# Optimization experiments

Measured on AMD Instinct MI355X. Metric: run time of the kernel, lower is better.

The kernel has to match this reference:

```python
import jax, jax.numpy as jnp
import numpy as np

NEG_INF = -1e30
LRELU_SLOPE = 0.2

B, E, IN_DIM, OUT_DIM = 64, 512, 1024, 256


def setup_inputs() -> dict:
    key = jax.random.key(0)
    ks = jax.random.split(key, 6)
    input_state = jax.random.normal(ks[0], (B, E, IN_DIM), dtype=jnp.float32)
    adj = jnp.ones((B, E, E), dtype=jnp.float32)  # only used via ones_like in the original
    node_mask = jax.random.randint(ks[1], (B, E, 1), 0, 2, dtype=jnp.int32)
    W_w = jax.random.normal(ks[2], (OUT_DIM, IN_DIM), dtype=jnp.float32) * (1.0 / np.sqrt(IN_DIM))
    W_b = jax.random.normal(ks[3], (OUT_DIM,), dtype=jnp.float32) * 0.02
    a_w = jax.random.normal(ks[4], (1, 2 * OUT_DIM), dtype=jnp.float32) * (1.0 / np.sqrt(2 * OUT_DIM))
    a_b = jax.random.normal(ks[5], (1,), dtype=jnp.float32) * 0.02
    return {"input_state": input_state, "adj": adj, "node_mask": node_mask,
            "W_w": W_w, "W_b": W_b, "a_w": a_w, "a_b": a_b}


def reference(input_state, adj, node_mask, W_w, W_b, a_w, a_b):
    # h = W(input_state); dropout is identity in eval mode (gnn_drop=0)
    h = jnp.einsum('bei,oi->beo', input_state, W_w) + W_b  # b,E,d
    d = h.shape[-1]
    # a([h_i ; h_j]) decomposes exactly: a_w[:, :d] @ h_i + a_w[:, d:] @ h_j + a_b
    a1, a2 = a_w[:, :d], a_w[:, d:]
    s1 = jnp.einsum('beo,xo->bex', h, a1)  # b,E,1 -> score contribution of source node i
    s2 = jnp.einsum('beo,xo->bex', h, a2)  # b,E,1 -> contribution of target node j
    scores = s1 + jnp.swapaxes(s2, 1, 2) + a_b  # b,E,E, scores[n,i,j] = a([h_i;h_j])
    scores = jnp.where(scores >= 0, scores, LRELU_SLOPE * scores)  # LeakyReLU(0.2)
    # fully-connected adjacency gated by node mask: mask_i * mask_j
    m = node_mask.astype(scores.dtype)  # b,E,1
    pair_mask = m * jnp.swapaxes(m, 1, 2)  # b,E,E
    scores = jnp.where(pair_mask > 0, scores, NEG_INF)
    coefs = jax.nn.softmax(scores, axis=-1)  # b,E,E
    h = h * m  # zero out masked nodes before aggregation
    return jnp.einsum('bij,bjo->bio', coefs, h)
```

## Files before the change

### kernel.cpp

```cpp
#include <hip/hip_runtime.h>
#include <hip/hip_fp16.h>
#include <math.h>

#define NEG_INF_F (-1e30f)
#define LRELU 0.2f

constexpr int Bb = 64, Ee = 512, IND = 1024, OUTD = 256;
constexpr int Mrows = Bb * Ee;

typedef __attribute__((ext_vector_type(8))) _Float16 half8;
typedef __attribute__((ext_vector_type(4))) _Float16 half4;
typedef __attribute__((ext_vector_type(4))) float floatx4;

#define AS1 __attribute__((address_space(1)))
#define AS3 __attribute__((address_space(3)))

__global__ __launch_bounds__(256) void wconv_kernel(
    const float* __restrict__ W, _Float16* __restrict__ Whf)
{
    const int i = (blockIdx.x * 256 + threadIdx.x) * 4;
    const float4 w = *reinterpret_cast<const float4*>(&W[i]);
    half4 hh;
    hh[0] = (_Float16)w.x; hh[1] = (_Float16)w.y;
    hh[2] = (_Float16)w.z; hh[3] = (_Float16)w.w;
    *reinterpret_cast<half4*>(&Whf[i]) = hh;
}

__global__ __launch_bounds__(256) void gemm_h_f16(
    const float* __restrict__ X, const _Float16* __restrict__ Whf,
    const float* __restrict__ Wb, const float* __restrict__ aw,
    const int* __restrict__ mask,
    _Float16* __restrict__ HmTh, _Float16* __restrict__ HmTl,
    float* __restrict__ s1, float* __restrict__ s2)
{
    __shared__ char lds_raw[81920];
    _Float16* As = (_Float16*)lds_raw;
    _Float16* Bs = (_Float16*)(lds_raw + 16384);
    float*    s1p  = (float*)lds_raw;
    float*    s2p  = (float*)(lds_raw + 1024);
    float*    mkfs = (float*)(lds_raw + 2048);
    _Float16* Th   = (_Float16*)(lds_raw + 16384);
    _Float16* Tl   = (_Float16*)(lds_raw + 49152);

    const int t  = threadIdx.x;
    const int w  = t >> 6;
    const int l  = t & 63;
    const int ln = l & 15;
    const int lg = l >> 4;
    const int m0 = blockIdx.x * 64;

    const int mA = t >> 3, pp = t & 7;
    const int aswz = pp ^ (mA & 7);
    const float* __restrict__ xbase = X + (size_t)m0 * IND;

    const int bn_sub = l >> 3;
    const int bkg = (l & 7) ^ (bn_sub & 7);

    floatx4 acc[4][4];
    #pragma unroll
    for (int i = 0; i < 4; ++i)
        #pragma unroll
        for (int j = 0; j < 4; ++j)
            acc[i][j] = (floatx4)0.f;

    auto loadA = [&](int k0, float4 xr[2][2]) {
        #pragma unroll
        for (int i = 0; i < 2; ++i) {
            const float* p = xbase + (size_t)(mA + 32 * i) * IND + k0 + pp * 8;
            xr[i][0] = *reinterpret_cast<const float4*>(p);
            xr[i][1] = *reinterpret_cast<const float4*>(p + 4);
        }
    };
    auto writeA = [&](int buf, float4 xr[2][2]) {
        #pragma unroll
        for (int i = 0; i < 2; ++i) {
            half8 h;
            h[0] = (_Float16)xr[i][0].x; h[1] = (_Float16)xr[i][0].y;
            h[2] = (_Float16)xr[i][0].z; h[3] = (_Float16)xr[i][0].w;
            h[4] = (_Float16)xr[i][1].x; h[5] = (_Float16)xr[i][1].y;
            h[6] = (_Float16)xr[i][1].z; h[7] = (_Float16)xr[i][1].w;
            *reinterpret_cast<half8*>(As + buf * 4096 + (mA + 32 * i) * 64 + aswz * 8) = h;
        }
    };
    auto stageB = [&](int buf, int k0) {
        #pragma unroll
        for (int j = 0; j < 8; ++j) {
            const int n = w * 64 + j * 8 + bn_sub;
            __builtin_amdgcn_global_load_lds(
                (const AS1 unsigned int*)(Whf + (size_t)n * IND + k0 + bkg * 8),
                (AS3 unsigned int*)(Bs + buf * 16384 + w * 4096 + j * 512),
                16, 0, 0);
        }
    };

    {
        float4 xr[2][2];
        loadA(0, xr);
        stageB(0, 0);
        writeA(0, xr);
    }
    __syncthreads();

    #pragma unroll 2
    for (int step = 0; step < 16; ++step) {
        const int buf = step & 1;
        float4 xn[2][2];
        if (step < 15) {
            loadA((step + 1) * 64, xn);
            stageB(buf ^ 1, (step + 1) * 64);
        }

        half8 af[2][4], bf[2][4];
        #pragma unroll
        for (int kk = 0; kk < 2; ++kk) {
            #pragma unroll
            for (int mr = 0; mr < 4; ++mr) {
                const int row = mr * 16 + ln;
                const int ch = (kk * 4 + lg) ^ (ln & 7);
                af[kk][mr] = *reinterpret_cast<const half8*>(As + buf * 4096 + row * 64 + ch * 8);
            }
            #pragma unroll
            for (int nr = 0; nr < 4; ++nr) {
                const int n = w * 64 + nr * 16 + ln;
                const int ch = (kk * 4 + lg) ^ (ln & 7);
                bf[kk][nr] = *reinterpret_cast<const half8*>(Bs + buf * 16384 + n * 64 + ch * 8);
            }
        }
        #pragma unroll
        for (int kk = 0; kk < 2; ++kk)
            #pragma unroll
            for (int mr = 0; mr < 4; ++mr)
                #pragma unroll
                for (int nr = 0; nr < 4; ++nr)
                    acc[mr][nr] = __builtin_amdgcn_mfma_f32_16x16x32_f16(
                        af[kk][mr], bf[kk][nr], acc[mr][nr], 0, 0, 0);

        if (step < 15) writeA(buf ^ 1, xn);
        __syncthreads();
    }

    if (t < 64) mkfs[t] = (float)mask[m0 + t];
    __syncthreads();

    float bias[4], a1c[4], a2c[4];
    #pragma unroll
    for (int nr = 0; nr < 4; ++nr) {
        const int n = w * 64 + nr * 16 + ln;
        bias[nr] = Wb[n];
        a1c[nr]  = aw[n];
        a2c[nr]  = aw[OUTD + n];
    }
    float sv1[4][4], sv2[4][4];
    #pragma unroll
    for (int i = 0; i < 4; ++i)
        #pragma unroll
        for (int r = 0; r < 4; ++r) { sv1[i][r] = 0.f; sv2[i][r] = 0.f; }

    #pragma unroll
    for (int mr = 0; mr < 4; ++mr)
        #pragma unroll
        for (int nr = 0; nr < 4; ++nr) {
            const int n = w * 64 + nr * 16 + ln;
            half4 hh, hl;
            #pragma unroll
            for (int rr = 0; rr < 4; ++rr) {
                const float hb = acc[mr][nr][rr] + bias[nr];
                sv1[mr][rr] += hb * a1c[nr];
                sv2[mr][rr] += hb * a2c[nr];
                const float hm = hb * mkfs[mr * 16 + lg * 4 + rr];
                const _Float16 hhi = (_Float16)hm;
                hh[rr] = hhi;
                hl[rr] = (_Float16)(hm - (float)hhi);
            }
            const int idx = n * 64 + ((mr * 16 + lg * 4) ^ ((n & 7) << 3));
            *reinterpret_cast<half4*>(Th + idx) = hh;
            *reinterpret_cast<half4*>(Tl + idx) = hl;
        }

    #pragma unroll
    for (int mr = 0; mr < 4; ++mr)
        #pragma unroll
        for (int rr = 0; rr < 4; ++rr) {
            float v1 = sv1[mr][rr], v2 = sv2[mr][rr];
            #pragma unroll
            for (int off = 1; off < 16; off <<= 1) {
                v1 += __shfl_xor(v1, off, 64);
                v2 += __shfl_xor(v2, off, 64);
            }
            if (ln == 0) {
                s1p[w * 64 + mr * 16 + lg * 4 + rr] = v1;
                s2p[w * 64 + mr * 16 + lg * 4 + rr] = v2;
            }
        }
    __syncthreads();

    if (t < 64) {
        s1[m0 + t] = s1p[t] + s1p[64 + t] + s1p[128 + t] + s1p[192 + t];
        s2[m0 + t] = s2p[t] + s2p[64 + t] + s2p[128 + t] + s2p[192 + t];
    }

    const int bIdx = m0 >> 9;
    const int e0   = m0 & 511;
    #pragma unroll
    for (int r4 = 0; r4 < 16; ++r4) {
        const int o = w * 64 + r4 * 4 + lg;
        const int src = o * 64 + ((ln * 4) ^ ((o & 7) << 3));
        const half4 vh = *reinterpret_cast<const half4*>(Th + src);
        const half4 vl = *reinterpret_cast<const half4*>(Tl + src);
        const size_t goff = ((size_t)(bIdx * OUTD + o) << 9) + e0 + ln * 4;
        *reinterpret_cast<half4*>(&HmTh[goff]) = vh;
        *reinterpret_cast<half4*>(&HmTl[goff]) = vl;
    }
}

__global__ __launch_bounds__(256, 2) void attn_mfma(
    const _Float16* __restrict__ HmTh, const _Float16* __restrict__ HmTl,
    const float* __restrict__ s1, const float* __restrict__ s2,
    const int* __restrict__ mask, const float* __restrict__ ab_ptr,
    float* __restrict__ Out)
{
    __shared__ float s2v[Ee];
    __shared__ float mkv[Ee];
    __shared__ float rowc[64];
    __shared__ float rmax[64];
    __shared__ int   rvv[64];
    __shared__ _Float16 Pl[2][64][32];
    __shared__ float Zp[64][4];
    __shared__ float zr[64];
    __shared__ float wmax[4];

    const int bid = blockIdx.x;
    const int b  = bid & 63;
    const int i0 = (bid >> 6) * 64;
    const int t  = threadIdx.x;
    const int w  = t >> 6, l = t & 63, ln = l & 15, lg = l >> 4;
    const float ab = ab_ptr[0];

    float lmax = -INFINITY;
    #pragma unroll
    for (int q = 0; q < 2; ++q) {
        const int j = t + q * 256;
        const float sv = s2[b * Ee + j];
        const float mv = (float)mask[b * Ee + j];
        s2v[j] = sv; mkv[j] = mv;
        if (mv > 0.f) lmax = fmaxf(lmax, sv);
    }
    #pragma unroll
    for (int off = 32; off; off >>= 1) lmax = fmaxf(lmax, __shfl_xor(lmax, off, 64));
    if (l == 0) wmax[w] = lmax;
    __syncthreads();
    const float s2max = fmaxf(fmaxf(wmax[0], wmax[1]), fmaxf(wmax[2], wmax[3]));
    const int anyvalid = (s2max > -1e37f) ? 1 : 0;
    if (t < 64) {
        const float c = s1[b * Ee + i0 + t] + ab;
        rowc[t] = c;
        const int mi = mask[b * Ee + i0 + t];
        rvv[t] = (mi != 0) & anyvalid;
        const float rm = c + s2max;
        rmax[t] = (rm >= 0.f) ? rm : LRELU * rm;
    }
    __syncthreads();

    const int pi = t >> 2;
    const int pj = (t & 3) * 8;
    const float prc = rowc[pi];
    const float prm = rmax[pi];
    const int   prv = rvv[pi];
    float zacc = 0.f;

    const size_t obase = (size_t)b * OUTD * Ee;
    const int o0 = w * 64;

    floatx4 acc[4][4];
    #pragma unroll
    for (int i = 0; i < 4; ++i)
        #pragma unroll
        for (int j = 0; j < 4; ++j)
            acc[i][j] = (floatx4)0.f;

    for (int ks = 0; ks < 16; ++ks) {
        const int k0  = ks * 32;
        const int buf = ks & 1;

        half8 ph;
        #pragma unroll
        for (int kk = 0; kk < 8; ++kk) {
            const int j = k0 + pj + kk;
            float pv;
            if (prv) {
                float sc = prc + s2v[j];
                sc = (sc >= 0.f) ? sc : LRELU * sc;
                pv = (mkv[j] > 0.f) ? __expf(sc - prm) : 0.f;
            } else {
                pv = 1.f;
            }
            const _Float16 hq = (_Float16)pv;
            ph[kk] = hq;
            zacc += (float)hq;
        }
        *reinterpret_cast<half8*>(&Pl[buf][pi][pj]) = ph;

        half8 bh[4], bl[4];
        #pragma unroll
        for (int ot = 0; ot < 4; ++ot) {
            const size_t ro = obase + (size_t)(o0 + ot * 16 + ln) * Ee + k0 + lg * 8;
            bh[ot] = *reinterpret_cast<const half8*>(&HmTh[ro]);
            bl[ot] = *reinterpret_cast<const half8*>(&HmTl[ro]);
        }
        __syncthreads();

        half8 af[4];
        #pragma unroll
        for (int mr = 0; mr < 4; ++mr)
            af[mr] = *reinterpret_cast<const half8*>(&Pl[buf][mr * 16 + ln][lg * 8]);
        #pragma unroll
        for (int mr = 0; mr < 4; ++mr)
            #pragma unroll
            for (int ot = 0; ot < 4; ++ot) {
                acc[mr][ot] = __builtin_amdgcn_mfma_f32_16x16x32_f16(
                    af[mr], bh[ot], acc[mr][ot], 0, 0, 0);
                acc[mr][ot] = __builtin_amdgcn_mfma_f32_16x16x32_f16(
                    af[mr], bl[ot], acc[mr][ot], 0, 0, 0);
            }
    }

    Zp[pi][t & 3] = zacc;
    __syncthreads();
    if (t < 64) {
        const float z = Zp[t][0] + Zp[t][1] + Zp[t][2] + Zp[t][3];
        zr[t] = 1.f / z;
    }
    __syncthreads();

    float* __restrict__ Ob = Out + ((size_t)b * Ee + i0) * OUTD;
    #pragma unroll
    for (int mr = 0; mr < 4; ++mr)
        #pragma unroll
        for (int rr = 0; rr < 4; ++rr) {
            const int i = mr * 16 + lg * 4 + rr;
            const float rzi = zr[i];
            #pragma unroll
            for (int ot = 0; ot < 4; ++ot)
                Ob[(size_t)i * OUTD + o0 + ot * 16 + ln] = acc[mr][ot][rr] * rzi;
        }
}

extern "C" void kernel_launch(void* const* d_in, const int* in_sizes, int n_in,
                              void* d_out, int out_size, void* d_ws, size_t ws_size,
                              hipStream_t stream) {
    const float* X    = (const float*)d_in[0];
    const int*   mask = (const int*)d_in[2];
    const float* Ww   = (const float*)d_in[3];
    const float* Wb   = (const float*)d_in[4];
    const float* aw   = (const float*)d_in[5];
    const float* ab   = (const float*)d_in[6];
    float* out = (float*)d_out;

    _Float16* HmTh = (_Float16*)d_ws;
    _Float16* HmTl = HmTh + (size_t)Bb * OUTD * Ee;
    float* s1 = (float*)(HmTl + (size_t)Bb * OUTD * Ee);
    float* s2 = s1 + Mrows;
    _Float16* Whf = (_Float16*)(s2 + Mrows);

    wconv_kernel<<<OUTD * IND / (256 * 4), 256, 0, stream>>>(Ww, Whf);
    gemm_h_f16<<<Mrows / 64, 256, 0, stream>>>(X, Whf, Wb, aw, mask,
                                               HmTh, HmTl, s1, s2);
    attn_mfma<<<Bb * (Ee / 64), 256, 0, stream>>>(HmTh, HmTl, s1, s2, mask, ab, out);
}
```

Before: 83.25 us.

## Drop hi/lo fp16 split of H and restructure GEMM with triple-buffered async loads

The projection GEMM now stages fp32 X tiles directly into LDS with global_load_lds and converts them to fp16 when reading fragments. It uses a three-stage ring of 32-wide K chunks with explicit waitcnt and barrier control, setprio around the MFMAs, and launch bounds of two blocks per SM. Separately, the low-half correction term of H is removed, which halves the transposed H writes and reads and the MFMAs in the attention kernel. The cost is lower accuracy, since H is now stored only as a single fp16 value.

```diff
diff --git a/kernel.cpp b/kernel.cpp
--- a/kernel.cpp
+++ b/kernel.cpp
@@ -26,35 +26,28 @@
     *reinterpret_cast<half4*>(&Whf[i]) = hh;
 }
 
-__global__ __launch_bounds__(256) void gemm_h_f16(
+__global__ __launch_bounds__(256, 2) void gemm_h_f16(
     const float* __restrict__ X, const _Float16* __restrict__ Whf,
     const float* __restrict__ Wb, const float* __restrict__ aw,
     const int* __restrict__ mask,
-    _Float16* __restrict__ HmTh, _Float16* __restrict__ HmTl,
-    float* __restrict__ s1, float* __restrict__ s2)
+    _Float16* __restrict__ HmTh, float* __restrict__ s1, float* __restrict__ s2)
 {
-    __shared__ char lds_raw[81920];
-    _Float16* As = (_Float16*)lds_raw;
-    _Float16* Bs = (_Float16*)(lds_raw + 16384);
-    float*    s1p  = (float*)lds_raw;
-    float*    s2p  = (float*)(lds_raw + 1024);
-    float*    mkfs = (float*)(lds_raw + 2048);
-    _Float16* Th   = (_Float16*)(lds_raw + 16384);
-    _Float16* Tl   = (_Float16*)(lds_raw + 49152);
+    __shared__ char lds_raw[73728];
+    float*    Af  = (float*)lds_raw;
+    _Float16* Bf  = (_Float16*)(lds_raw + 24576);
+    _Float16* Th   = (_Float16*)lds_raw;
+    float*    s1p  = (float*)(lds_raw + 32768);
+    float*    s2p  = (float*)(lds_raw + 33792);
+    float*    mkfs = (float*)(lds_raw + 34816);
 
     const int t  = threadIdx.x;
-    const int w  = t >> 6;
-    const int l  = t & 63;
-    const int ln = l & 15;
-    const int lg = l >> 4;
+    const int w  = t >> 6, l = t & 63, ln = l & 15, lg = l >> 4;
     const int m0 = blockIdx.x * 64;
 
-    const int mA = t >> 3, pp = t & 7;
-    const int aswz = pp ^ (mA & 7);
-    const float* __restrict__ xbase = X + (size_t)m0 * IND;
-
-    const int bn_sub = l >> 3;
-    const int bkg = (l & 7) ^ (bn_sub & 7);
+    const int arl = l >> 3;
+    const int agl = (l & 7) ^ arl;
+    const int brl = l >> 2;
+    const int bgl = (l & 3) ^ ((l >> 3) & 3);
 
     floatx4 acc[4][4];
     #pragma unroll
@@ -63,84 +56,84 @@
         for (int j = 0; j < 4; ++j)
             acc[i][j] = (floatx4)0.f;
 
-    auto loadA = [&](int k0, float4 xr[2][2]) {
+    auto stageA = [&](int kc, int aoff) {
         #pragma unroll
         for (int i = 0; i < 2; ++i) {
-            const float* p = xbase + (size_t)(mA + 32 * i) * IND + k0 + pp * 8;
-            xr[i][0] = *reinterpret_cast<const float4*>(p);
-            xr[i][1] = *reinterpret_cast<const float4*>(p + 4);
+            const int rbase = (w * 2 + i) * 8;
+            const size_t src = (size_t)(m0 + rbase + arl) * IND + kc * 32 + agl * 4;
+            __builtin_amdgcn_global_load_lds(
+                (const AS1 unsigned int*)(X + src),
+                (AS3 unsigned int*)(Af + aoff + rbase * 32), 16, 0, 0);
         }
     };
-    auto writeA = [&](int buf, float4 xr[2][2]) {
-        #pragma unroll
-        for (int i = 0; i < 2; ++i) {
+    auto stageB = [&](int kc, int boff) {
+        #pragma unroll
+        for (int i = 0; i < 4; ++i) {
+            const int nbase = w * 64 + i * 16;
+            const size_t src = (size_t)(nbase + brl) * IND + kc * 32 + bgl * 8;
+            __builtin_amdgcn_global_load_lds(
+                (const AS1 unsigned int*)(Whf + src),
+                (AS3 unsigned int*)(Bf + boff + nbase * 32), 16, 0, 0);
+        }
+    };
+
+    int aO0 = 0, aO1 = 2048, aO2 = 4096;
+    int bO0 = 0, bO1 = 8192, bO2 = 16384;
+
+    stageA(0, aO0); stageB(0, bO0);
+    stageA(1, aO1); stageB(1, bO1);
+    asm volatile("s_waitcnt vmcnt(6) lgkmcnt(0)" ::: "memory");
+    __builtin_amdgcn_sched_barrier(0);
+    __builtin_amdgcn_s_barrier();
+    __builtin_amdgcn_sched_barrier(0);
+
+    for (int ts = 0; ts < 32; ++ts) {
+        if (ts < 30) { stageA(ts + 2, aO2); stageB(ts + 2, bO2); }
+        __builtin_amdgcn_sched_barrier(0);
+
+        half8 bfrag[4];
+        #pragma unroll
+        for (int nr = 0; nr < 4; ++nr) {
+            const int n = w * 64 + nr * 16 + ln;
+            const int phys = lg ^ ((n >> 1) & 3);
+            bfrag[nr] = *reinterpret_cast<const half8*>(Bf + bO0 + n * 32 + phys * 8);
+        }
+        half8 afrag[4];
+        #pragma unroll
+        for (int mr = 0; mr < 4; ++mr) {
+            const int r = mr * 16 + ln;
+            const int g0 = (lg * 2) ^ (r & 7);
+            const int g1 = (lg * 2 + 1) ^ (r & 7);
+            const floatx4 a0 = *reinterpret_cast<const floatx4*>(Af + aO0 + r * 32 + g0 * 4);
+            const floatx4 a1 = *reinterpret_cast<const floatx4*>(Af + aO0 + r * 32 + g1 * 4);
             half8 h;
-            h[0] = (_Float16)xr[i][0].x; h[1] = (_Float16)xr[i][0].y;
-            h[2] = (_Float16)xr[i][0].z; h[3] = (_Float16)xr[i][0].w;
-            h[4] = (_Float16)xr[i][1].x; h[5] = (_Float16)xr[i][1].y;
-            h[6] = (_Float16)xr[i][1].z; h[7] = (_Float16)xr[i][1].w;
-            *reinterpret_cast<half8*>(As + buf * 4096 + (mA + 32 * i) * 64 + aswz * 8) = h;
-        }
-    };
-    auto stageB = [&](int buf, int k0) {
-        #pragma unroll
-        for (int j = 0; j < 8; ++j) {
-            const int n = w * 64 + j * 8 + bn_sub;
-            __builtin_amdgcn_global_load_lds(
-                (const AS1 unsigned int*)(Whf + (size_t)n * IND + k0 + bkg * 8),
-                (AS3 unsigned int*)(Bs + buf * 16384 + w * 4096 + j * 512),
-                16, 0, 0);
-        }
-    };
-
-    {
-        float4 xr[2][2];
-        loadA(0, xr);
-        stageB(0, 0);
-        writeA(0, xr);
-    }
-    __syncthreads();
-
-    #pragma unroll 2
-    for (int step = 0; step < 16; ++step) {
-        const int buf = step & 1;
-        float4 xn[2][2];
-        if (step < 15) {
-            loadA((step + 1) * 64, xn);
-            stageB(buf ^ 1, (step + 1) * 64);
-        }
-
-        half8 af[2][4], bf[2][4];
-        #pragma unroll
-        for (int kk = 0; kk < 2; ++kk) {
-            #pragma unroll
-            for (int mr = 0; mr < 4; ++mr) {
-                const int row = mr * 16 + ln;
-                const int ch = (kk * 4 + lg) ^ (ln & 7);
-                af[kk][mr] = *reinterpret_cast<const half8*>(As + buf * 4096 + row * 64 + ch * 8);
-            }
-            #pragma unroll
-            for (int nr = 0; nr < 4; ++nr) {
-                const int n = w * 64 + nr * 16 + ln;
-                const int ch = (kk * 4 + lg) ^ (ln & 7);
-                bf[kk][nr] = *reinterpret_cast<const half8*>(Bs + buf * 16384 + n * 64 + ch * 8);
-            }
-        }
-        #pragma unroll
-        for (int kk = 0; kk < 2; ++kk)
-            #pragma unroll
-            for (int mr = 0; mr < 4; ++mr)
-                #pragma unroll
-                for (int nr = 0; nr < 4; ++nr)
-                    acc[mr][nr] = __builtin_amdgcn_mfma_f32_16x16x32_f16(
-                        af[kk][mr], bf[kk][nr], acc[mr][nr], 0, 0, 0);
-
-        if (step < 15) writeA(buf ^ 1, xn);
-        __syncthreads();
+            h[0] = (_Float16)a0[0]; h[1] = (_Float16)a0[1];
+            h[2] = (_Float16)a0[2]; h[3] = (_Float16)a0[3];
+            h[4] = (_Float16)a1[0]; h[5] = (_Float16)a1[1];
+            h[6] = (_Float16)a1[2]; h[7] = (_Float16)a1[3];
+            afrag[mr] = h;
+        }
+
+        __builtin_amdgcn_s_setprio(1);
+        #pragma unroll
+        for (int mr = 0; mr < 4; ++mr)
+            #pragma unroll
+            for (int nr = 0; nr < 4; ++nr)
+                acc[mr][nr] = __builtin_amdgcn_mfma_f32_16x16x32_f16(
+                    afrag[mr], bfrag[nr], acc[mr][nr], 0, 0, 0);
+        __builtin_amdgcn_s_setprio(0);
+
+        if (ts < 29) asm volatile("s_waitcnt vmcnt(6) lgkmcnt(0)" ::: "memory");
+        else         asm volatile("s_waitcnt vmcnt(0) lgkmcnt(0)" ::: "memory");
+        __builtin_amdgcn_sched_barrier(0);
+        __builtin_amdgcn_s_barrier();
+        __builtin_amdgcn_sched_barrier(0);
+
+        int tmp = aO0; aO0 = aO1; aO1 = aO2; aO2 = tmp;
+        tmp = bO0; bO0 = bO1; bO1 = bO2; bO2 = tmp;
     }
 
     if (t < 64) mkfs[t] = (float)mask[m0 + t];
-    __syncthreads();
 
     float bias[4], a1c[4], a2c[4];
     #pragma unroll
@@ -160,21 +153,17 @@
     for (int mr = 0; mr < 4; ++mr)
         #pragma unroll
         for (int nr = 0; nr < 4; ++nr) {
-            const int n = w * 64 + nr * 16 + ln;
-            half4 hh, hl;
+            const int o = w * 64 + nr * 16 + ln;
+            half4 hh;
             #pragma unroll
             for (int rr = 0; rr < 4; ++rr) {
                 const float hb = acc[mr][nr][rr] + bias[nr];
                 sv1[mr][rr] += hb * a1c[nr];
                 sv2[mr][rr] += hb * a2c[nr];
-                const float hm = hb * mkfs[mr * 16 + lg * 4 + rr];
-                const _Float16 hhi = (_Float16)hm;
-                hh[rr] = hhi;
-                hl[rr] = (_Float16)(hm - (float)hhi);
+                hh[rr] = (_Float16)hb;
             }
-            const int idx = n * 64 + ((mr * 16 + lg * 4) ^ ((n & 7) << 3));
-            *reinterpret_cast<half4*>(Th + idx) = hh;
-            *reinterpret_cast<half4*>(Tl + idx) = hl;
+            const int e = mr * 16 + lg * 4;
+            *reinterpret_cast<half4*>(Th + o * 64 + (e ^ ((o & 7) << 3))) = hh;
         }
 
     #pragma unroll
@@ -188,8 +177,9 @@
                 v2 += __shfl_xor(v2, off, 64);
             }
             if (ln == 0) {
-                s1p[w * 64 + mr * 16 + lg * 4 + rr] = v1;
-                s2p[w * 64 + mr * 16 + lg * 4 + rr] = v2;
+                const int e = mr * 16 + lg * 4 + rr;
+                s1p[w * 64 + e] = v1;
+                s2p[w * 64 + e] = v2;
             }
         }
     __syncthreads();
@@ -201,20 +191,24 @@
 
     const int bIdx = m0 >> 9;
     const int e0   = m0 & 511;
-    #pragma unroll
-    for (int r4 = 0; r4 < 16; ++r4) {
-        const int o = w * 64 + r4 * 4 + lg;
-        const int src = o * 64 + ((ln * 4) ^ ((o & 7) << 3));
-        const half4 vh = *reinterpret_cast<const half4*>(Th + src);
-        const half4 vl = *reinterpret_cast<const half4*>(Tl + src);
-        const size_t goff = ((size_t)(bIdx * OUTD + o) << 9) + e0 + ln * 4;
+    const int e4   = (t & 15) * 4;
+    const float q0 = mkfs[e4 + 0], q1 = mkfs[e4 + 1];
+    const float q2 = mkfs[e4 + 2], q3 = mkfs[e4 + 3];
+    #pragma unroll
+    for (int it = 0; it < 16; ++it) {
+        const int o = it * 16 + (t >> 4);
+        half4 vh = *reinterpret_cast<const half4*>(Th + o * 64 + (e4 ^ ((o & 7) << 3)));
+        if (!(q0 > 0.f)) vh[0] = (_Float16)0.f;
+        if (!(q1 > 0.f)) vh[1] = (_Float16)0.f;
+        if (!(q2 > 0.f)) vh[2] = (_Float16)0.f;
+        if (!(q3 > 0.f)) vh[3] = (_Float16)0.f;
+        const size_t goff = ((size_t)(bIdx * OUTD + o) << 9) + e0 + e4;
         *reinterpret_cast<half4*>(&HmTh[goff]) = vh;
-        *reinterpret_cast<half4*>(&HmTl[goff]) = vl;
     }
 }
 
 __global__ __launch_bounds__(256, 2) void attn_mfma(
-    const _Float16* __restrict__ HmTh, const _Float16* __restrict__ HmTl,
+    const _Float16* __restrict__ HmTh,
     const float* __restrict__ s1, const float* __restrict__ s2,
     const int* __restrict__ mask, const float* __restrict__ ab_ptr,
     float* __restrict__ Out)
@@ -300,12 +294,11 @@
         }
         *reinterpret_cast<half8*>(&Pl[buf][pi][pj]) = ph;
 
-        half8 bh[4], bl[4];
+        half8 bh[4];
         #pragma unroll
         for (int ot = 0; ot < 4; ++ot) {
             const size_t ro = obase + (size_t)(o0 + ot * 16 + ln) * Ee + k0 + lg * 8;
             bh[ot] = *reinterpret_cast<const half8*>(&HmTh[ro]);
-            bl[ot] = *reinterpret_cast<const half8*>(&HmTl[ro]);
         }
         __syncthreads();
 
@@ -316,12 +309,9 @@
         #pragma unroll
         for (int mr = 0; mr < 4; ++mr)
             #pragma unroll
-            for (int ot = 0; ot < 4; ++ot) {
+            for (int ot = 0; ot < 4; ++ot)
                 acc[mr][ot] = __builtin_amdgcn_mfma_f32_16x16x32_f16(
                     af[mr], bh[ot], acc[mr][ot], 0, 0, 0);
-                acc[mr][ot] = __builtin_amdgcn_mfma_f32_16x16x32_f16(
-                    af[mr], bl[ot], acc[mr][ot], 0, 0, 0);
-            }
     }
 
     Zp[pi][t & 3] = zacc;
@@ -357,13 +347,11 @@
     float* out = (float*)d_out;
 
     _Float16* HmTh = (_Float16*)d_ws;
-    _Float16* HmTl = HmTh + (size_t)Bb * OUTD * Ee;
-    float* s1 = (float*)(HmTl + (size_t)Bb * OUTD * Ee);
+    float* s1 = (float*)(HmTh + (size_t)Bb * OUTD * Ee);
     float* s2 = s1 + Mrows;
     _Float16* Whf = (_Float16*)(s2 + Mrows);
 
     wconv_kernel<<<OUTD * IND / (256 * 4), 256, 0, stream>>>(Ww, Whf);
-    gemm_h_f16<<<Mrows / 64, 256, 0, stream>>>(X, Whf, Wb, aw, mask,
-                                               HmTh, HmTl, s1, s2);
-    attn_mfma<<<Bb * (Ee / 64), 256, 0, stream>>>(HmTh, HmTl, s1, s2, mask, ab, out);
+    gemm_h_f16<<<Mrows / 64, 256, 0, stream>>>(X, Whf, Wb, aw, mask, HmTh, s1, s2);
+    attn_mfma<<<Bb * (Ee / 64), 256, 0, stream>>>(HmTh, s1, s2, mask, ab, out);
 }
```

Result: faster. 73.31 us (-11.9%).
